# Kernel tuning notes

Measured on AMD Instinct MI355X. Metric: run time of the kernel, lower is better.

## Reference

```python
import jax, jax.numpy as jnp
import numpy as np

M, A, N, Bb, RANK = 64, 64, 64, 64, 2  # d_in = N*Bb = 4096, d_out = M*A = 4096
TOKENS = 16384


def setup_inputs() -> dict:
    key = jax.random.key(0)
    k1, k2, k3, k4 = jax.random.split(key, 4)
    x = jax.random.normal(k1, (TOKENS, N * Bb), dtype=jnp.float32)
    btt_l = jax.random.normal(k2, (M, N * RANK, A), dtype=jnp.float32)
    btt_r = jax.random.normal(k3, (N, Bb, M * RANK), dtype=jnp.float32)
    bias = jax.random.normal(k4, (M * A,), dtype=jnp.float32)
    return {"x": x, "btt_l": btt_l, "btt_r": btt_r, "bias": bias}


def reference(x, btt_l, btt_r, bias):
    # Block tensor-train (BTT) factorized linear: y = BTT(btt_l, btt_r) @ x + bias
    B = x.shape[0]
    m, nr, a = btt_l.shape          # (M, N*RANK, A)
    n, b, mr = btt_r.shape          # (N, Bb, M*RANK)
    rank = nr // n
    # Stage 1: per n-block, map b -> m*rank
    h = jnp.einsum('tnb,nbk->tnk', x.reshape(B, n, b), btt_r)  # (B, n, m*rank)
    # Regroup: (B, n, m, rank) -> (B, m, n, rank) -> (B, m, n*rank)
    h = h.reshape(B, n, m, rank).transpose(0, 2, 1, 3).reshape(B, m, n * rank)
    # Stage 2: per m-block, map n*rank -> a
    y = jnp.einsum('tmj,mja->tma', h, btt_l).reshape(B, m * a)
    return y + bias
```

## Files before the change

kernel.cpp:

```cpp
#include <hip/hip_runtime.h>
#include <hip/hip_bf16.h>

typedef __attribute__((ext_vector_type(8))) short short8;
typedef __attribute__((ext_vector_type(4))) float f32x4;
typedef __attribute__((ext_vector_type(4))) unsigned int u32x4;
typedef __attribute__((ext_vector_type(2))) unsigned int u32x2;

#define DIN  4096
#define DOUT 4096
#define NTOK 16384

static __device__ __forceinline__ unsigned short f2b(float f) {
  union { __hip_bfloat16 h; unsigned short u; } cv;
  cv.h = __float2bfloat16(f);
  return cv.u;
}

static __device__ __forceinline__ short8 pack8(float4 f0, float4 f1) {
  short8 s;
  s[0] = (short)f2b(f0.x); s[1] = (short)f2b(f0.y);
  s[2] = (short)f2b(f0.z); s[3] = (short)f2b(f0.w);
  s[4] = (short)f2b(f1.x); s[5] = (short)f2b(f1.y);
  s[6] = (short)f2b(f1.z); s[7] = (short)f2b(f1.w);
  return s;
}

__global__ __launch_bounds__(256) void prep(const float* __restrict__ r,
                                            const float* __restrict__ l,
                                            unsigned short* __restrict__ rt,
                                            unsigned short* __restrict__ lt) {
  __shared__ unsigned short tile[128 * 68];
  const int q = threadIdx.x;
  if (blockIdx.x < 64) {
    const int n = blockIdx.x;
#pragma unroll
    for (int it = 0; it < 8; ++it) {
      const int idx = q + it * 256;
      const int b = idx >> 5, k4 = idx & 31;
      const float4 v = *(const float4*)(r + (size_t)n * 8192 + b * 128 + k4 * 4);
      unsigned int lo = (unsigned)f2b(v.x) | ((unsigned)f2b(v.y) << 16);
      unsigned int hi = (unsigned)f2b(v.z) | ((unsigned)f2b(v.w) << 16);
      u32x2 pk = {lo, hi};
      *(u32x2*)((char*)tile + (b * 264 + k4 * 8)) = pk;
    }
    __syncthreads();
#pragma unroll
    for (int it = 0; it < 32; ++it) {
      const int o = q + it * 256;
      const int c = o >> 6, b = o & 63;
      rt[(size_t)n * 8192 + o] = tile[b * 132 + c];
    }
  } else {
    const int m = blockIdx.x - 64;
#pragma unroll
    for (int it = 0; it < 8; ++it) {
      const int idx = q + it * 256;
      const int j = idx >> 4, a4 = idx & 15;
      const float4 v = *(const float4*)(l + (size_t)m * 8192 + j * 64 + a4 * 4);
      unsigned int lo = (unsigned)f2b(v.x) | ((unsigned)f2b(v.y) << 16);
      unsigned int hi = (unsigned)f2b(v.z) | ((unsigned)f2b(v.w) << 16);
      u32x2 pk = {lo, hi};
      *(u32x2*)((char*)tile + (j * 136 + a4 * 8)) = pk;
    }
    __syncthreads();
#pragma unroll
    for (int it = 0; it < 32; ++it) {
      const int o = q + it * 256;
      const int a = o >> 7, j = o & 127;
      lt[(size_t)m * 8192 + o] = tile[j * 68 + a];
    }
  }
}

__global__ __launch_bounds__(256) void k1(const float* __restrict__ x,
                                          const unsigned short* __restrict__ rt,
                                          unsigned short* __restrict__ hbuf,
                                          int tok0) {
  const int n = blockIdx.y;
  const int strip = blockIdx.x;
  const int wave = threadIdx.x >> 6, lane = threadIdx.x & 63;
  const int l15 = lane & 15, l4 = lane >> 4;

  short8 bf[8][2];
  {
    const unsigned short* rbase = rt + (size_t)n * 8192 + l15 * 64 + l4 * 8;
#pragma unroll
    for (int ct = 0; ct < 8; ++ct)
#pragma unroll
      for (int ks = 0; ks < 2; ++ks)
        bf[ct][ks] = *(const short8*)(rbase + ct * 1024 + ks * 32);
  }

  for (int tt = 0; tt < 4; ++tt) {
    const int tile = strip * 16 + tt * 4 + wave;
    const float* xr = x + (size_t)(tok0 + tile * 16 + l15) * DIN + n * 64 + l4 * 8;
    const float4 f0 = *(const float4*)(xr);
    const float4 f1 = *(const float4*)(xr + 4);
    const float4 g0 = *(const float4*)(xr + 32);
    const float4 g1 = *(const float4*)(xr + 36);
    const short8 a0 = pack8(f0, f1);
    const short8 a1 = pack8(g0, g1);
    unsigned short* hb = hbuf + (size_t)(tile * 64 + n) * 2048 + l15 * 16 + l4 * 4;
#pragma unroll
    for (int ct = 0; ct < 8; ++ct) {
      f32x4 acc = {0.f, 0.f, 0.f, 0.f};
      acc = __builtin_amdgcn_mfma_f32_16x16x32_bf16(a0, bf[ct][0], acc, 0, 0, 0);
      acc = __builtin_amdgcn_mfma_f32_16x16x32_bf16(a1, bf[ct][1], acc, 0, 0, 0);
      unsigned int lo = (unsigned)f2b(acc[0]) | ((unsigned)f2b(acc[1]) << 16);
      unsigned int hi = (unsigned)f2b(acc[2]) | ((unsigned)f2b(acc[3]) << 16);
      u32x2 pk = {lo, hi};
      *(u32x2*)(hb + ct * 256) = pk;
    }
  }
}

__global__ __launch_bounds__(256) void k2(const unsigned short* __restrict__ hbuf,
                                          const unsigned short* __restrict__ lt,
                                          const float* __restrict__ bias,
                                          float* __restrict__ y,
                                          int tok0) {
  __shared__ unsigned short as_[2][32 * 128];
  const int m = blockIdx.y;
  const int strip = blockIdx.x;
  const int tid = threadIdx.x;
  const int wave = tid >> 6, lane = tid & 63;
  const int l15 = lane & 15, l4 = lane >> 4;

  short8 bfr[4];
  {
    const unsigned short* lbase = lt + (size_t)m * 8192 + (wave * 16 + l15) * 128 + l4 * 8;
#pragma unroll
    for (int ks = 0; ks < 4; ++ks) bfr[ks] = *(const short8*)(lbase + ks * 32);
  }
  const int acol = wave * 16 + l15;
  const float bv = bias[m * 64 + acol];

  auto stage = [&](int it, int b) {
#pragma unroll
    for (int half = 0; half < 2; ++half) {
      const int idx = tid + half * 256;
      const int hh = idx & 1, nr = (idx >> 1) & 127, tio = idx >> 8;
      const int nn = nr >> 1, r2 = nr & 1;
      const int tg16 = strip * 16 + it * 2 + tio;
      const u32x4 v = *(const u32x4*)(hbuf + (size_t)(tg16 * 64 + nn) * 2048 +
                                      (m * 2 + r2) * 16 + hh * 8);
#pragma unroll
      for (int e = 0; e < 8; ++e) {
        const unsigned int w = v[e >> 1];
        const unsigned short val = (e & 1) ? (unsigned short)(w >> 16)
                                           : (unsigned short)(w & 0xffff);
        const int t = tio * 16 + hh * 8 + e;
        *(unsigned short*)((char*)as_[b] + (t * 256 + ((nr * 2) ^ ((t & 7) << 4)))) = val;
      }
    }
  };

  stage(0, 0);
  __syncthreads();
  int buf = 0;
  for (int it = 0; it < 8; ++it) {
    if (it + 1 < 8) stage(it + 1, buf ^ 1);
#pragma unroll
    for (int th = 0; th < 2; ++th) {
      const int ta = th * 16 + l15;
      f32x4 acc = {0.f, 0.f, 0.f, 0.f};
#pragma unroll
      for (int ks = 0; ks < 4; ++ks) {
        const short8 av = *(const short8*)((char*)as_[buf] +
                            (ta * 256 + ((ks * 64 + l4 * 16) ^ ((ta & 7) << 4))));
        acc = __builtin_amdgcn_mfma_f32_16x16x32_bf16(av, bfr[ks], acc, 0, 0, 0);
      }
      const size_t t0 = (size_t)(tok0 + strip * 256 + it * 32 + th * 16 + l4 * 4);
#pragma unroll
      for (int jj = 0; jj < 4; ++jj)
        y[(t0 + jj) * DOUT + m * 64 + acol] = acc[jj] + bv;
    }
    __syncthreads();
    buf ^= 1;
  }
}

extern "C" void kernel_launch(void* const* d_in, const int* in_sizes, int n_in,
                              void* d_out, int out_size, void* d_ws, size_t ws_size,
                              hipStream_t stream) {
  const float* x    = (const float*)d_in[0];
  const float* bl   = (const float*)d_in[1];
  const float* br   = (const float*)d_in[2];
  const float* bias = (const float*)d_in[3];
  float* y = (float*)d_out;

  unsigned short* rt   = (unsigned short*)d_ws;
  unsigned short* ltw  = rt + 64 * 8192;
  unsigned short* hbuf = ltw + 64 * 8192;

  const size_t fixed = (size_t)2 * 64 * 8192 * 2;
  int chunk = 4096;
  while (chunk > 256 && fixed + (size_t)chunk * 8192 * 2 > ws_size) chunk >>= 1;
  const int nchunk = NTOK / chunk;
  const int strips = chunk / 256;

  prep<<<128, 256, 0, stream>>>(br, bl, rt, ltw);
  for (int c = 0; c < nchunk; ++c) {
    k1<<<dim3(strips, 64), 256, 0, stream>>>(x, rt, hbuf, c * chunk);
    k2<<<dim3(strips, 64), 256, 0, stream>>>(hbuf, ltw, bias, y, c * chunk);
  }
}
```

Baseline: 298.9 us.

## Prefetch x tiles in k1 and pair m-blocks per k2 block for wider reads

k1 now double-buffers its per-wave x loads in registers, issuing the next tile's loads before converting and multiplying the current one, to hide global load latency. k2 is restructured so each block handles two adjacent m-blocks over 128 tokens. Each wave covers one m with two 16-column a-tiles, and the staging reads 128 contiguous bytes of hbuf per (token, n) row instead of 64. This is meant to improve hbuf read coalescing and MFMA density per LDS load, at the cost of doubling LDS use and the grid reshaping into fewer, larger blocks.

```diff
diff --git a/kernel.cpp b/kernel.cpp
--- a/kernel.cpp
+++ b/kernel.cpp
@@ -91,15 +91,23 @@
         bf[ct][ks] = *(const short8*)(rbase + ct * 1024 + ks * 32);
   }
 
+  const float* xb = x + (size_t)(tok0 + (strip * 16 + wave) * 16 + l15) * DIN
+                      + n * 64 + l4 * 8;
+  float4 p0[4], p1[4];
+  p0[0] = *(const float4*)(xb);      p0[1] = *(const float4*)(xb + 4);
+  p0[2] = *(const float4*)(xb + 32); p0[3] = *(const float4*)(xb + 36);
+#pragma unroll
   for (int tt = 0; tt < 4; ++tt) {
+    if (tt < 3) {
+      const float* xn = xb + (size_t)(tt + 1) * 4 * 16 * DIN;
+      float4* dst = (tt & 1) ? p0 : p1;
+      dst[0] = *(const float4*)(xn);      dst[1] = *(const float4*)(xn + 4);
+      dst[2] = *(const float4*)(xn + 32); dst[3] = *(const float4*)(xn + 36);
+    }
+    const float4* cur = (tt & 1) ? p1 : p0;
+    const short8 a0 = pack8(cur[0], cur[1]);
+    const short8 a1 = pack8(cur[2], cur[3]);
     const int tile = strip * 16 + tt * 4 + wave;
-    const float* xr = x + (size_t)(tok0 + tile * 16 + l15) * DIN + n * 64 + l4 * 8;
-    const float4 f0 = *(const float4*)(xr);
-    const float4 f1 = *(const float4*)(xr + 4);
-    const float4 g0 = *(const float4*)(xr + 32);
-    const float4 g1 = *(const float4*)(xr + 36);
-    const short8 a0 = pack8(f0, f1);
-    const short8 a1 = pack8(g0, g1);
     unsigned short* hb = hbuf + (size_t)(tile * 64 + n) * 2048 + l15 * 16 + l4 * 4;
 #pragma unroll
     for (int ct = 0; ct < 8; ++ct) {
@@ -119,38 +127,43 @@
                                           const float* __restrict__ bias,
                                           float* __restrict__ y,
                                           int tok0) {
-  __shared__ unsigned short as_[2][32 * 128];
-  const int m = blockIdx.y;
+  __shared__ unsigned short as_[2][2][32 * 128];
+  const int mp = blockIdx.y;
   const int strip = blockIdx.x;
   const int tid = threadIdx.x;
   const int wave = tid >> 6, lane = tid & 63;
   const int l15 = lane & 15, l4 = lane >> 4;
-
-  short8 bfr[4];
-  {
-    const unsigned short* lbase = lt + (size_t)m * 8192 + (wave * 16 + l15) * 128 + l4 * 8;
-#pragma unroll
-    for (int ks = 0; ks < 4; ++ks) bfr[ks] = *(const short8*)(lbase + ks * 32);
-  }
-  const int acol = wave * 16 + l15;
-  const float bv = bias[m * 64 + acol];
+  const int m_loc = wave & 1, ah = wave >> 1;
+  const int m = mp * 2 + m_loc;
+
+  short8 bfr[2][4];
+#pragma unroll
+  for (int at = 0; at < 2; ++at)
+#pragma unroll
+    for (int ks = 0; ks < 4; ++ks)
+      bfr[at][ks] = *(const short8*)(lt + (size_t)m * 8192 +
+                      (ah * 32 + at * 16 + l15) * 128 + ks * 32 + l4 * 8);
+  const float bv0 = bias[m * 64 + ah * 32 + l15];
+  const float bv1 = bias[m * 64 + ah * 32 + 16 + l15];
 
   auto stage = [&](int it, int b) {
 #pragma unroll
-    for (int half = 0; half < 2; ++half) {
+    for (int half = 0; half < 4; ++half) {
       const int idx = tid + half * 256;
-      const int hh = idx & 1, nr = (idx >> 1) & 127, tio = idx >> 8;
-      const int nn = nr >> 1, r2 = nr & 1;
-      const int tg16 = strip * 16 + it * 2 + tio;
+      const int sub8 = idx & 7, nn = (idx >> 3) & 63, tio = idx >> 9;
+      const int tg16 = strip * 8 + it * 2 + tio;
       const u32x4 v = *(const u32x4*)(hbuf + (size_t)(tg16 * 64 + nn) * 2048 +
-                                      (m * 2 + r2) * 16 + hh * 8);
+                                      mp * 64 + sub8 * 8);
+      const int c_loc = sub8 >> 1, hh = sub8 & 1;
+      const int j = nn * 2 + (c_loc & 1), ml = c_loc >> 1;
+      char* base = (char*)as_ + ((b * 2 + ml) * 32) * 256;
 #pragma unroll
       for (int e = 0; e < 8; ++e) {
         const unsigned int w = v[e >> 1];
         const unsigned short val = (e & 1) ? (unsigned short)(w >> 16)
                                            : (unsigned short)(w & 0xffff);
         const int t = tio * 16 + hh * 8 + e;
-        *(unsigned short*)((char*)as_[b] + (t * 256 + ((nr * 2) ^ ((t & 7) << 4)))) = val;
+        *(unsigned short*)(base + t * 256 + ((j * 2) ^ ((t & 7) << 4))) = val;
       }
     }
   };
@@ -158,22 +171,34 @@
   stage(0, 0);
   __syncthreads();
   int buf = 0;
-  for (int it = 0; it < 8; ++it) {
-    if (it + 1 < 8) stage(it + 1, buf ^ 1);
+  for (int it = 0; it < 4; ++it) {
+    if (it < 3) stage(it + 1, buf ^ 1);
+    f32x4 acc00 = {0,0,0,0}, acc01 = {0,0,0,0}, acc10 = {0,0,0,0}, acc11 = {0,0,0,0};
+    const char* abase = (char*)as_ + ((buf * 2 + m_loc) * 32) * 256;
 #pragma unroll
     for (int th = 0; th < 2; ++th) {
-      const int ta = th * 16 + l15;
-      f32x4 acc = {0.f, 0.f, 0.f, 0.f};
+      const int t = th * 16 + l15;
 #pragma unroll
       for (int ks = 0; ks < 4; ++ks) {
-        const short8 av = *(const short8*)((char*)as_[buf] +
-                            (ta * 256 + ((ks * 64 + l4 * 16) ^ ((ta & 7) << 4))));
-        acc = __builtin_amdgcn_mfma_f32_16x16x32_bf16(av, bfr[ks], acc, 0, 0, 0);
+        const short8 av = *(const short8*)(abase + t * 256 +
+                            ((ks * 64 + l4 * 16) ^ ((t & 7) << 4)));
+        if (th == 0) {
+          acc00 = __builtin_amdgcn_mfma_f32_16x16x32_bf16(av, bfr[0][ks], acc00, 0, 0, 0);
+          acc10 = __builtin_amdgcn_mfma_f32_16x16x32_bf16(av, bfr[1][ks], acc10, 0, 0, 0);
+        } else {
+          acc01 = __builtin_amdgcn_mfma_f32_16x16x32_bf16(av, bfr[0][ks], acc01, 0, 0, 0);
+          acc11 = __builtin_amdgcn_mfma_f32_16x16x32_bf16(av, bfr[1][ks], acc11, 0, 0, 0);
+        }
       }
-      const size_t t0 = (size_t)(tok0 + strip * 256 + it * 32 + th * 16 + l4 * 4);
-#pragma unroll
-      for (int jj = 0; jj < 4; ++jj)
-        y[(t0 + jj) * DOUT + m * 64 + acol] = acc[jj] + bv;
+    }
+    const size_t t0 = (size_t)(tok0 + strip * 128 + it * 32 + l4 * 4);
+    float* y0 = y + (size_t)m * 64 + ah * 32 + l15;
+#pragma unroll
+    for (int jj = 0; jj < 4; ++jj) {
+      y0[(t0 + jj) * DOUT]      = acc00[jj] + bv0;
+      y0[(t0 + jj) * DOUT + 16] = acc10[jj] + bv1;
+      y0[(t0 + 16 + jj) * DOUT]      = acc01[jj] + bv0;
+      y0[(t0 + 16 + jj) * DOUT + 16] = acc11[jj] + bv1;
     }
     __syncthreads();
     buf ^= 1;
@@ -197,11 +222,10 @@
   int chunk = 4096;
   while (chunk > 256 && fixed + (size_t)chunk * 8192 * 2 > ws_size) chunk >>= 1;
   const int nchunk = NTOK / chunk;
-  const int strips = chunk / 256;
 
   prep<<<128, 256, 0, stream>>>(br, bl, rt, ltw);
   for (int c = 0; c < nchunk; ++c) {
-    k1<<<dim3(strips, 64), 256, 0, stream>>>(x, rt, hbuf, c * chunk);
-    k2<<<dim3(strips, 64), 256, 0, stream>>>(hbuf, ltw, bias, y, c * chunk);
-  }
-}
+    k1<<<dim3(chunk / 256, 64), 256, 0, stream>>>(x, rt, hbuf, c * chunk);
+    k2<<<dim3(chunk / 128, 32), 256, 0, stream>>>(hbuf, ltw, bias, y, c * chunk);
+  }
+}
```

Measured after the change: 293.2 us. No clear change (-1.9%).

## Fuse both BTT stages into one kernel with intermediate kept in LDS

Applied to the files above, without the earlier changes.

Replaces the two-kernel pipeline, which wrote the intermediate h to a global workspace in chunks, with a single fused kernel. Each 512-thread block handles 16 tokens, computes stage 1 into a swizzled LDS buffer, then accumulates stage 2 over four groups of 16 n-blocks, double-buffering x loads in registers across groups. This removes the global round trip of the intermediate and the per-chunk launches. In exchange, weight fragments are re-read from global or L2 by every block, and there are only 1024 blocks holding large register accumulators, which may limit occupancy.

```diff
diff --git a/kernel.cpp b/kernel.cpp
--- a/kernel.cpp
+++ b/kernel.cpp
@@ -3,7 +3,6 @@
 
 typedef __attribute__((ext_vector_type(8))) short short8;
 typedef __attribute__((ext_vector_type(4))) float f32x4;
-typedef __attribute__((ext_vector_type(4))) unsigned int u32x4;
 typedef __attribute__((ext_vector_type(2))) unsigned int u32x2;
 
 #define DIN  4096
@@ -72,112 +71,119 @@
   }
 }
 
-__global__ __launch_bounds__(256) void k1(const float* __restrict__ x,
-                                          const unsigned short* __restrict__ rt,
-                                          unsigned short* __restrict__ hbuf,
-                                          int tok0) {
-  const int n = blockIdx.y;
-  const int strip = blockIdx.x;
-  const int wave = threadIdx.x >> 6, lane = threadIdx.x & 63;
+__global__ __launch_bounds__(512) void fused(const float* __restrict__ x,
+                                             const unsigned short* __restrict__ rt,
+                                             const unsigned short* __restrict__ lt,
+                                             const float* __restrict__ bias,
+                                             float* __restrict__ y) {
+  __shared__ unsigned short hlds[32768];
+  const int t0 = blockIdx.x * 16;
+  const int tid = threadIdx.x, w = tid >> 6, lane = tid & 63;
   const int l15 = lane & 15, l4 = lane >> 4;
 
-  short8 bf[8][2];
-  {
-    const unsigned short* rbase = rt + (size_t)n * 8192 + l15 * 64 + l4 * 8;
-#pragma unroll
-    for (int ct = 0; ct < 8; ++ct)
+  const float* xrow = x + (size_t)(t0 + l15) * DIN + l4 * 8;
+
+  f32x4 acc[8][4];
+#pragma unroll
+  for (int mi = 0; mi < 8; ++mi)
+#pragma unroll
+    for (int at = 0; at < 4; ++at) acc[mi][at] = (f32x4){0.f, 0.f, 0.f, 0.f};
+
+  float4 xA[2][2][2], xB[2][2][2];
+
+  auto LOADX = [&](int g, float4 (&xb)[2][2][2]) {
+#pragma unroll
+    for (int np = 0; np < 2; ++np) {
+      const float* p = xrow + (size_t)(g * 16 + w * 2 + np) * 64;
 #pragma unroll
       for (int ks = 0; ks < 2; ++ks)
-        bf[ct][ks] = *(const short8*)(rbase + ct * 1024 + ks * 32);
+#pragma unroll
+        for (int h = 0; h < 2; ++h)
+          xb[np][ks][h] = *(const float4*)(p + ks * 32 + h * 4);
+    }
+  };
+
+  auto STAGE1 = [&](int g, float4 (&xb)[2][2][2]) {
+#pragma unroll
+    for (int np = 0; np < 2; ++np) {
+      const int n = g * 16 + w * 2 + np;
+      const int nl = w * 2 + np;
+      const short8 xf0 = pack8(xb[np][0][0], xb[np][0][1]);
+      const short8 xf1 = pack8(xb[np][1][0], xb[np][1][1]);
+      const unsigned short* rb = rt + (size_t)n * 8192 + l15 * 64 + l4 * 8;
+#pragma unroll
+      for (int ct = 0; ct < 8; ++ct) {
+        const short8 r0 = *(const short8*)(rb + ct * 1024);
+        const short8 r1 = *(const short8*)(rb + ct * 1024 + 32);
+        f32x4 s = {0.f, 0.f, 0.f, 0.f};
+        s = __builtin_amdgcn_mfma_f32_16x16x32_bf16(r0, xf0, s, 0, 0, 0);
+        s = __builtin_amdgcn_mfma_f32_16x16x32_bf16(r1, xf1, s, 0, 0, 0);
+        const int m0 = ct * 8 + l4 * 2;
+#pragma unroll
+        for (int dd = 0; dd < 2; ++dd) {
+          const int m = m0 + dd;
+          const unsigned int pk =
+              (unsigned)f2b(s[2 * dd]) | ((unsigned)f2b(s[2 * dd + 1]) << 16);
+          int byte = nl * 4096 + m * 64 + l15 * 4;
+          byte ^= ((((m >> 1) ^ (nl >> 2)) & 1) << 6);
+          *(unsigned int*)((char*)hlds + byte) = pk;
+        }
+      }
+    }
+  };
+
+  auto STAGE2 = [&](int g) {
+#pragma unroll
+    for (int mi = 0; mi < 8; ++mi) {
+      const int m = w * 8 + mi;
+      union { unsigned int u[4]; short8 s; } hu;
+#pragma unroll
+      for (int q = 0; q < 4; ++q) {
+        const int nl = l4 * 4 + q;
+        int byte = nl * 4096 + m * 64 + l15 * 4;
+        byte ^= ((((m >> 1) ^ (nl >> 2)) & 1) << 6);
+        hu.u[q] = *(const unsigned int*)((char*)hlds + byte);
+      }
+      const unsigned short* lb = lt + (size_t)m * 8192 + l15 * 128 + g * 32 + l4 * 8;
+#pragma unroll
+      for (int at = 0; at < 4; ++at) {
+        const short8 lf = *(const short8*)(lb + at * 2048);
+        acc[mi][at] =
+            __builtin_amdgcn_mfma_f32_16x16x32_bf16(lf, hu.s, acc[mi][at], 0, 0, 0);
+      }
+    }
+  };
+
+#define BARRIER()                                          \
+  do {                                                     \
+    asm volatile("s_waitcnt lgkmcnt(0)" ::: "memory");     \
+    __builtin_amdgcn_s_barrier();                          \
+    asm volatile("" ::: "memory");                         \
+  } while (0)
+
+  LOADX(0, xA);
+  LOADX(1, xB); STAGE1(0, xA); BARRIER(); STAGE2(0); BARRIER();
+  LOADX(2, xA); STAGE1(1, xB); BARRIER(); STAGE2(1); BARRIER();
+  LOADX(3, xB); STAGE1(2, xA); BARRIER(); STAGE2(2); BARRIER();
+                STAGE1(3, xB); BARRIER(); STAGE2(3);
+
+#pragma unroll
+  for (int mi = 0; mi < 8; ++mi) {
+    const int m = w * 8 + mi;
+    float* yb = y + (size_t)(t0 + l15) * DOUT + m * 64 + l4 * 4;
+    const float* bb = bias + m * 64 + l4 * 4;
+#pragma unroll
+    for (int at = 0; at < 4; ++at) {
+      const float4 bv = *(const float4*)(bb + at * 16);
+      float4 o;
+      o.x = acc[mi][at][0] + bv.x;
+      o.y = acc[mi][at][1] + bv.y;
+      o.z = acc[mi][at][2] + bv.z;
+      o.w = acc[mi][at][3] + bv.w;
+      *(float4*)(yb + at * 16) = o;
+    }
   }
-
-  for (int tt = 0; tt < 4; ++tt) {
-    const int tile = strip * 16 + tt * 4 + wave;
-    const float* xr = x + (size_t)(tok0 + tile * 16 + l15) * DIN + n * 64 + l4 * 8;
-    const float4 f0 = *(const float4*)(xr);
-    const float4 f1 = *(const float4*)(xr + 4);
-    const float4 g0 = *(const float4*)(xr + 32);
-    const float4 g1 = *(const float4*)(xr + 36);
-    const short8 a0 = pack8(f0, f1);
-    const short8 a1 = pack8(g0, g1);
-    unsigned short* hb = hbuf + (size_t)(tile * 64 + n) * 2048 + l15 * 16 + l4 * 4;
-#pragma unroll
-    for (int ct = 0; ct < 8; ++ct) {
-      f32x4 acc = {0.f, 0.f, 0.f, 0.f};
-      acc = __builtin_amdgcn_mfma_f32_16x16x32_bf16(a0, bf[ct][0], acc, 0, 0, 0);
-      acc = __builtin_amdgcn_mfma_f32_16x16x32_bf16(a1, bf[ct][1], acc, 0, 0, 0);
-      unsigned int lo = (unsigned)f2b(acc[0]) | ((unsigned)f2b(acc[1]) << 16);
-      unsigned int hi = (unsigned)f2b(acc[2]) | ((unsigned)f2b(acc[3]) << 16);
-      u32x2 pk = {lo, hi};
-      *(u32x2*)(hb + ct * 256) = pk;
-    }
-  }
-}
-
-__global__ __launch_bounds__(256) void k2(const unsigned short* __restrict__ hbuf,
-                                          const unsigned short* __restrict__ lt,
-                                          const float* __restrict__ bias,
-                                          float* __restrict__ y,
-                                          int tok0) {
-  __shared__ unsigned short as_[2][32 * 128];
-  const int m = blockIdx.y;
-  const int strip = blockIdx.x;
-  const int tid = threadIdx.x;
-  const int wave = tid >> 6, lane = tid & 63;
-  const int l15 = lane & 15, l4 = lane >> 4;
-
-  short8 bfr[4];
-  {
-    const unsigned short* lbase = lt + (size_t)m * 8192 + (wave * 16 + l15) * 128 + l4 * 8;
-#pragma unroll
-    for (int ks = 0; ks < 4; ++ks) bfr[ks] = *(const short8*)(lbase + ks * 32);
-  }
-  const int acol = wave * 16 + l15;
-  const float bv = bias[m * 64 + acol];
-
-  auto stage = [&](int it, int b) {
-#pragma unroll
-    for (int half = 0; half < 2; ++half) {
-      const int idx = tid + half * 256;
-      const int hh = idx & 1, nr = (idx >> 1) & 127, tio = idx >> 8;
-      const int nn = nr >> 1, r2 = nr & 1;
-      const int tg16 = strip * 16 + it * 2 + tio;
-      const u32x4 v = *(const u32x4*)(hbuf + (size_t)(tg16 * 64 + nn) * 2048 +
-                                      (m * 2 + r2) * 16 + hh * 8);
-#pragma unroll
-      for (int e = 0; e < 8; ++e) {
-        const unsigned int w = v[e >> 1];
-        const unsigned short val = (e & 1) ? (unsigned short)(w >> 16)
-                                           : (unsigned short)(w & 0xffff);
-        const int t = tio * 16 + hh * 8 + e;
-        *(unsigned short*)((char*)as_[b] + (t * 256 + ((nr * 2) ^ ((t & 7) << 4)))) = val;
-      }
-    }
-  };
-
-  stage(0, 0);
-  __syncthreads();
-  int buf = 0;
-  for (int it = 0; it < 8; ++it) {
-    if (it + 1 < 8) stage(it + 1, buf ^ 1);
-#pragma unroll
-    for (int th = 0; th < 2; ++th) {
-      const int ta = th * 16 + l15;
-      f32x4 acc = {0.f, 0.f, 0.f, 0.f};
-#pragma unroll
-      for (int ks = 0; ks < 4; ++ks) {
-        const short8 av = *(const short8*)((char*)as_[buf] +
-                            (ta * 256 + ((ks * 64 + l4 * 16) ^ ((ta & 7) << 4))));
-        acc = __builtin_amdgcn_mfma_f32_16x16x32_bf16(av, bfr[ks], acc, 0, 0, 0);
-      }
-      const size_t t0 = (size_t)(tok0 + strip * 256 + it * 32 + th * 16 + l4 * 4);
-#pragma unroll
-      for (int jj = 0; jj < 4; ++jj)
-        y[(t0 + jj) * DOUT + m * 64 + acol] = acc[jj] + bv;
-    }
-    __syncthreads();
-    buf ^= 1;
-  }
+#undef BARRIER
 }
 
 extern "C" void kernel_launch(void* const* d_in, const int* in_sizes, int n_in,
@@ -189,19 +195,9 @@
   const float* bias = (const float*)d_in[3];
   float* y = (float*)d_out;
 
-  unsigned short* rt   = (unsigned short*)d_ws;
-  unsigned short* ltw  = rt + 64 * 8192;
-  unsigned short* hbuf = ltw + 64 * 8192;
-
-  const size_t fixed = (size_t)2 * 64 * 8192 * 2;
-  int chunk = 4096;
-  while (chunk > 256 && fixed + (size_t)chunk * 8192 * 2 > ws_size) chunk >>= 1;
-  const int nchunk = NTOK / chunk;
-  const int strips = chunk / 256;
+  unsigned short* rt  = (unsigned short*)d_ws;
+  unsigned short* ltw = rt + 64 * 8192;
 
   prep<<<128, 256, 0, stream>>>(br, bl, rt, ltw);
-  for (int c = 0; c < nchunk; ++c) {
-    k1<<<dim3(strips, 64), 256, 0, stream>>>(x, rt, hbuf, c * chunk);
-    k2<<<dim3(strips, 64), 256, 0, stream>>>(hbuf, ltw, bias, y, c * chunk);
-  }
-}
+  fused<<<NTOK / 16, 512, 0, stream>>>(x, rt, ltw, bias, y);
+}
```

Result: slower. 444.8 us (+48.8%).
